# Kernel optimization log

Measured on AMD Instinct MI355X. Metric: run time of the kernel, lower is better.

Reference implementation:

```python
import jax, jax.numpy as jnp
import numpy as np
from jax import lax

K = 3        # kernel_size
PAD = 1      # padding
STRIDE = 1   # stride


def conv2d(x, w, stride, pad):
    return lax.conv_general_dilated(
        x, w, (stride, stride), [(pad, pad), (pad, pad)],
        dimension_numbers=('NCHW', 'OIHW', 'NCHW'))


def setup_inputs() -> dict:
    key = jax.random.key(0)
    ks = jax.random.split(key, 8)
    B, Ci, Cc, H, W = 8, 64, 64, 128, 128
    K2 = K * K
    return {
        'x_img': jax.random.normal(ks[0], (B, Ci, H, W), jnp.float32),
        'x_cont': jax.random.normal(ks[1], (B, Cc, H, W), jnp.float32),
        'w_fuse': jax.random.normal(ks[2], (Ci, Ci + Cc, 1, 1), jnp.float32) * 0.05,
        'w_off': jax.random.normal(ks[3], (2 * K2, Ci, K, K), jnp.float32) * 0.01,
        'b_off': jax.random.normal(ks[4], (2 * K2,), jnp.float32) * 0.1,
        'w_mod': jax.random.normal(ks[5], (K2, Ci, K, K), jnp.float32) * 0.01,
        'b_mod': jax.random.normal(ks[6], (K2,), jnp.float32) * 0.1,
        'w_reg': jax.random.normal(ks[7], (Ci, Ci, K, K), jnp.float32) * 0.05,
    }


def _bilinear_sample(img, py, px):
    # Zero padding outside the image (per-corner validity, matches torchvision).
    C, Hin, Win = img.shape
    flat = img.reshape(C, -1)
    y0 = jnp.floor(py)
    x0 = jnp.floor(px)

    def gather(yy, xx):
        valid = (yy >= 0) & (yy <= Hin - 1) & (xx >= 0) & (xx <= Win - 1)
        yc = jnp.clip(yy, 0, Hin - 1).astype(jnp.int32)
        xc = jnp.clip(xx, 0, Win - 1).astype(jnp.int32)
        return flat[:, yc * Win + xc] * valid[None].astype(img.dtype)

    wy1 = py - y0; wy0 = 1.0 - wy1
    wx1 = px - x0; wx0 = 1.0 - wx1
    return (gather(y0, x0) * (wy0 * wx0)[None]
            + gather(y0, x0 + 1.0) * (wy0 * wx1)[None]
            + gather(y0 + 1.0, x0) * (wy1 * wx0)[None]
            + gather(y0 + 1.0, x0 + 1.0) * (wy1 * wx1)[None])


def reference(x_img, x_cont, w_fuse, w_off, b_off, w_mod, b_mod, w_reg):
    # 1x1 fuse of image features with control factor
    x = conv2d(jnp.concatenate([x_img, x_cont], axis=1), w_fuse, 1, 0)
    # offset / modulator branches
    off = conv2d(x, w_off, STRIDE, PAD) + b_off[None, :, None, None]
    mod = 2.0 * jax.nn.sigmoid(conv2d(x, w_mod, STRIDE, PAD) + b_mod[None, :, None, None])
    B, C, Hin, Win = x.shape
    K2 = K * K
    Hout, Wout = off.shape[2], off.shape[3]
    # torchvision layout: channel 2k = dy, 2k+1 = dx for kernel pos k = i*K + j
    off = off.reshape(B, K2, 2, Hout, Wout)
    dy, dx = off[:, :, 0], off[:, :, 1]
    ky = (jnp.arange(K2) // K).astype(x.dtype)
    kx = (jnp.arange(K2) % K).astype(x.dtype)
    base_y = (jnp.arange(Hout) * STRIDE - PAD).astype(x.dtype)
    base_x = (jnp.arange(Wout) * STRIDE - PAD).astype(x.dtype)
    py = dy + base_y[None, None, :, None] + ky[None, :, None, None]  # [B,K2,H,W]
    px = dx + base_x[None, None, None, :] + kx[None, :, None, None]
    sampled = jax.vmap(_bilinear_sample)(x, py, px)          # [B,C,K2,H,W]
    sampled = sampled * mod[:, None]                          # modulation
    out = jnp.einsum('oik,bikhw->bohw', w_reg.reshape(C, C, K2), sampled)
    return out
```

## Files before the change

### kernel.cpp

```cpp
#include <hip/hip_runtime.h>
#include <math.h>

#define B_   8
#define C_   64
#define H_   128
#define W_   128
#define HW_  16384
#define K2_  9

typedef float f32x4 __attribute__((ext_vector_type(4)));
typedef short bf16x8 __attribute__((ext_vector_type(8)));
typedef unsigned short u16x4 __attribute__((ext_vector_type(4)));

#define WS_WRP  8192
#define WS_WRP2 26624
#define WS_XT   45056
#define WS_OM   8433664

static __device__ __forceinline__ unsigned short f2bf(float x) {
    unsigned int u = __float_as_uint(x);
    unsigned int r = (u + 0x7fffu + ((u >> 16) & 1u)) >> 16;
    return (unsigned short)r;
}
static __device__ __forceinline__ float bf2f(unsigned short u) {
    return __uint_as_float(((unsigned int)u) << 16);
}

__global__ __launch_bounds__(256) void k_fuse(const float* __restrict__ xi,
                                              const float* __restrict__ xc,
                                              const float* __restrict__ wf,
                                              const float* __restrict__ wreg,
                                              const float* __restrict__ wOff,
                                              const float* __restrict__ wMod,
                                              unsigned short* __restrict__ xtb,
                                              unsigned short* __restrict__ wrP,
                                              unsigned short* __restrict__ wrP2) {
    __shared__ unsigned short sA[1024 * 8];
    const int t = threadIdx.x;
    const int lane = t & 63;
    const int wv = t >> 6;
    const int b = blockIdx.x & 7;
    const int yh = blockIdx.x >> 3;
    const int y = yh >> 1;
    const int h = yh & 1;

    if (blockIdx.x < 18) {
        const int idx = blockIdx.x * 256 + t;
        if (idx < 4608) {
            int ln = idx & 63, mt = (idx >> 6) & 3, kc = (idx >> 8) & 1, tap = idx >> 9;
            int o = mt * 16 + (ln & 15);
            int ibase = kc * 32 + (ln >> 4) * 8;
#pragma unroll
            for (int j = 0; j < 8; ++j)
                wrP[idx * 8 + j] = f2bf(wreg[(o * 64 + ibase + j) * 9 + tap]);
        }
        if (idx < 2304) {
            int ln = idx & 63, mt = (idx >> 6) & 1, kc = idx >> 7;
            int m = mt * 16 + (ln & 15);
            int gkb = kc * 32 + (ln >> 4) * 8;
#pragma unroll
            for (int j = 0; j < 8; ++j) {
                int gk = gkb + j, tap = gk >> 6, ci = gk & 63;
                float v = 0.f;
                if (m < 18)      v = wOff[(m * 64 + ci) * 9 + tap];
                else if (m < 27) v = wMod[((m - 18) * 64 + ci) * 9 + tap];
                wrP2[idx * 8 + j] = f2bf(v);
            }
        }
    }

#pragma unroll
    for (int r = 0; r < 4; ++r) {
        const int c = t + 256 * r;
        const int f = c >> 6;
        const int ln = c & 63;
        const int mt = f & 3, kc = f >> 2;
        const int m = mt * 16 + (ln & 15);
        const int kb = kc * 32 + (ln >> 4) * 8;
        const float* s = wf + m * 128 + kb;
        unsigned short us[8];
#pragma unroll
        for (int j = 0; j < 8; ++j) us[j] = f2bf(s[j]);
        *(bf16x8*)&sA[c * 8] = *(const bf16x8*)us;
    }
    __syncthreads();

    const int n15 = lane & 15;
    const int q4 = lane >> 4;
    const int px = h * 64 + wv * 16 + n15;
    const size_t poff = (size_t)y * W_ + px;

    f32x4 acc[4];
#pragma unroll
    for (int mt = 0; mt < 4; ++mt) acc[mt] = (f32x4){0.f, 0.f, 0.f, 0.f};

#pragma unroll
    for (int kc = 0; kc < 4; ++kc) {
        const float* src = (kc < 2)
            ? (xi + ((size_t)(b * 64 + kc * 32 + q4 * 8)) * HW_ + poff)
            : (xc + ((size_t)(b * 64 + (kc - 2) * 32 + q4 * 8)) * HW_ + poff);
        unsigned short us[8];
#pragma unroll
        for (int j = 0; j < 8; ++j) us[j] = f2bf(src[(size_t)j * HW_]);
        const bf16x8 bf = *(const bf16x8*)us;
#pragma unroll
        for (int mt = 0; mt < 4; ++mt) {
            const bf16x8 a = *(const bf16x8*)&sA[((kc * 4 + mt) * 64 + lane) * 8];
            acc[mt] = __builtin_amdgcn_mfma_f32_16x16x32_bf16(a, bf, acc[mt], 0, 0, 0);
        }
    }

#pragma unroll
    for (int mt = 0; mt < 4; ++mt) {
        u16x4 o4;
        o4.x = f2bf(acc[mt][0]); o4.y = f2bf(acc[mt][1]);
        o4.z = f2bf(acc[mt][2]); o4.w = f2bf(acc[mt][3]);
        *(u16x4*)&xtb[((size_t)b * HW_ + poff) * 64 + mt * 16 + q4 * 4] = o4;
    }
}

__global__ __launch_bounds__(256) void k_offmod(const unsigned short* __restrict__ xtb,
                                                const unsigned short* __restrict__ wrP2,
                                                const float* __restrict__ bOff,
                                                const float* __restrict__ bMod,
                                                float* __restrict__ om) {
    __shared__ unsigned short sB[3 * 66 * 72];
    const int t = threadIdx.x;
    const int lane = t & 63;
    const int wv = t >> 6;
    const int b = blockIdx.x & 7;
    const int yh = blockIdx.x >> 3;
    const int y = yh >> 1;
    const int h = yh & 1;

    for (int idx = t; idx < 3 * 66 * 8; idx += 256) {
        const int c8 = idx & 7;
        const int pp = (idx >> 3) % 66;
        const int row = (idx >> 3) / 66;
        const int gx = h * 64 + pp - 1;
        const int gy = y + row - 1;
        bf16x8 v = {0, 0, 0, 0, 0, 0, 0, 0};
        if (gx >= 0 && gx < W_ && gy >= 0 && gy < H_)
            v = *(const bf16x8*)&xtb[(((size_t)(b * H_ + gy)) * W_ + gx) * 64 + c8 * 8];
        *(bf16x8*)&sB[(row * 66 + pp) * 72 + c8 * 8] = v;
    }
    __syncthreads();

    const int n15 = lane & 15;
    const int q4 = lane >> 4;

    f32x4 acc[2];
    acc[0] = (f32x4){0.f, 0.f, 0.f, 0.f};
    acc[1] = (f32x4){0.f, 0.f, 0.f, 0.f};

#pragma unroll
    for (int kc = 0; kc < 18; ++kc) {
        const int gkb = kc * 32 + q4 * 8;
        const int tap = gkb >> 6;
        const int ci = gkb & 63;
        const int row = tap / 3, kx = tap % 3;
        const bf16x8 bf = *(const bf16x8*)&sB[(row * 66 + (wv * 16 + n15 + kx)) * 72 + ci];
        const bf16x8 a0 = *(const bf16x8*)(wrP2 + (((size_t)(kc * 2 + 0) * 64 + lane) * 8));
        const bf16x8 a1 = *(const bf16x8*)(wrP2 + (((size_t)(kc * 2 + 1) * 64 + lane) * 8));
        acc[0] = __builtin_amdgcn_mfma_f32_16x16x32_bf16(a0, bf, acc[0], 0, 0, 0);
        acc[1] = __builtin_amdgcn_mfma_f32_16x16x32_bf16(a1, bf, acc[1], 0, 0, 0);
    }

    const int px = h * 64 + wv * 16 + n15;
    const size_t rec = ((size_t)(b * H_ + y)) * 28 * 128;
#pragma unroll
    for (int mt = 0; mt < 2; ++mt)
#pragma unroll
        for (int r = 0; r < 4; ++r) {
            const int o = mt * 16 + q4 * 4 + r;
            if (o < 18) {
                const int c = (o >> 1) + ((o & 1) ? 9 : 0);
                om[rec + c * 128 + px] = acc[mt][r] + bOff[o];
            } else if (o < 27) {
                const float z = acc[mt][r] + bMod[o - 18];
                om[rec + (18 + (o - 18)) * 128 + px] = 2.f / (1.f + __expf(-z));
            }
        }
}

__global__ __launch_bounds__(256) void k_deform(const unsigned short* __restrict__ xtb,
                                                const float* __restrict__ om,
                                                const unsigned short* __restrict__ wrP,
                                                float* __restrict__ out) {
    __shared__ unsigned short sS2[8 * 520];
    const int t = threadIdx.x;
    const int lane = t & 63;
    const int wv = t >> 6;
    const int b = blockIdx.x & 7;
    const int yh = blockIdx.x >> 3;
    const int y = yh >> 1;
    const int h = yh & 1;

    const char* xbB = (const char*)(xtb + (size_t)b * HW_ * 64);
    const float* omr = om + ((size_t)(b * H_ + y)) * 28 * 128;

    const int n15 = lane & 15;
    const int q4 = lane >> 4;
    const int pA = lane >> 2;
    const int corner = lane & 3;
    const int cy = corner >> 1, cx = corner & 1;
    const int pxA = h * 64 + wv * 16 + pA;
    const int gwrite = (lane >> 3) * 520 + (lane & 7);

    f32x4 acc[4];
#pragma unroll
    for (int mt = 0; mt < 4; ++mt) acc[mt] = (f32x4){0.f, 0.f, 0.f, 0.f};

    for (int k = 0; k < 9; ++k) {
        const int ky = k / 3 - 1, kx = k % 3 - 1;

        int rOff;
        int rW;
        {
            const float dy = omr[k * 128 + pxA];
            const float dxv = omr[(9 + k) * 128 + pxA];
            const float m = omr[(18 + k) * 128 + pxA];
            const float py  = (float)(y + ky) + dy;
            const float pxe = (float)(pxA + kx) + dxv;
            const float y0f = floorf(py), x0f = floorf(pxe);
            const int y0i = (int)y0f, x0i = (int)x0f;
            const float wy1 = py - y0f, wx1 = pxe - x0f;
            const int yy = y0i + cy;
            const int xx = x0i + cx;
            const bool ok = (yy >= 0) && (yy < H_) && (xx >= 0) && (xx < W_);
            const int yc = min(max(yy, 0), H_ - 1);
            const int xc = min(max(xx, 0), W_ - 1);
            const float w = (cy ? wy1 : 1.f - wy1) * (cx ? wx1 : 1.f - wx1) * m;
            rOff = (yc * W_ + xc) * 128;
            rW = (int)__float_as_uint(ok ? w : 0.f);
        }

#pragma unroll
        for (int p = 0; p < 16; ++p) {
            const int l0 = p * 4;
            const unsigned o0 = (unsigned)__builtin_amdgcn_readlane(rOff, l0 + 0);
            const unsigned o1 = (unsigned)__builtin_amdgcn_readlane(rOff, l0 + 1);
            const unsigned o2 = (unsigned)__builtin_amdgcn_readlane(rOff, l0 + 2);
            const unsigned o3 = (unsigned)__builtin_amdgcn_readlane(rOff, l0 + 3);
            const float w0 = __uint_as_float((unsigned)__builtin_amdgcn_readlane(rW, l0 + 0));
            const float w1 = __uint_as_float((unsigned)__builtin_amdgcn_readlane(rW, l0 + 1));
            const float w2 = __uint_as_float((unsigned)__builtin_amdgcn_readlane(rW, l0 + 2));
            const float w3 = __uint_as_float((unsigned)__builtin_amdgcn_readlane(rW, l0 + 3));
            const unsigned short* b0 = (const unsigned short*)(xbB + o0);
            const unsigned short* b1 = (const unsigned short*)(xbB + o1);
            const unsigned short* b2 = (const unsigned short*)(xbB + o2);
            const unsigned short* b3 = (const unsigned short*)(xbB + o3);
            const float v = bf2f(b0[lane]) * w0 + bf2f(b1[lane]) * w1
                          + bf2f(b2[lane]) * w2 + bf2f(b3[lane]) * w3;
            sS2[gwrite + (wv * 16 + p) * 8] = f2bf(v);
        }

#pragma unroll
        for (int kc = 0; kc < 2; ++kc) {
            const bf16x8 bf = *(const bf16x8*)&sS2[(kc * 4 + q4) * 520 + (wv * 16 + n15) * 8];
#pragma unroll
            for (int mt = 0; mt < 4; ++mt) {
                const bf16x8 a = *(const bf16x8*)(wrP +
                    ((((size_t)((k * 2 + kc) * 4 + mt)) * 64 + lane) * 8));
                acc[mt] = __builtin_amdgcn_mfma_f32_16x16x32_bf16(a, bf, acc[mt], 0, 0, 0);
            }
        }
    }

    const int px = h * 64 + wv * 16 + n15;
#pragma unroll
    for (int mt = 0; mt < 4; ++mt)
#pragma unroll
        for (int r = 0; r < 4; ++r) {
            const int o = mt * 16 + q4 * 4 + r;
            out[(((size_t)(b * 64 + o)) * H_ + y) * W_ + px] = acc[mt][r];
        }
}

extern "C" void kernel_launch(void* const* d_in, const int* in_sizes, int n_in,
                              void* d_out, int out_size, void* d_ws, size_t ws_size,
                              hipStream_t stream) {
    const float* x_img  = (const float*)d_in[0];
    const float* x_cont = (const float*)d_in[1];
    const float* w_fuse = (const float*)d_in[2];
    const float* w_off  = (const float*)d_in[3];
    const float* b_off  = (const float*)d_in[4];
    const float* w_mod  = (const float*)d_in[5];
    const float* b_mod  = (const float*)d_in[6];
    const float* w_reg  = (const float*)d_in[7];
    float* out = (float*)d_out;

    float* ws  = (float*)d_ws;
    unsigned short* wrP  = (unsigned short*)(ws + WS_WRP);
    unsigned short* wrP2 = (unsigned short*)(ws + WS_WRP2);
    unsigned short* xtb  = (unsigned short*)(ws + WS_XT);
    float* om  = ws + WS_OM;

    k_fuse<<<B_ * H_ * 2, 256, 0, stream>>>(x_img, x_cont, w_fuse, w_reg, w_off,
                                            w_mod, xtb, wrP, wrP2);
    k_offmod<<<B_ * H_ * 2, 256, 0, stream>>>(xtb, wrP2, b_off, b_mod, om);
    k_deform<<<B_ * H_ * 2, 256, 0, stream>>>(xtb, om, wrP, out);
}
```

Baseline: 215.7 us.

## Gather deformable samples directly into MFMA B-operand registers, dropping LDS staging

Rewrites the bilinear sampling in the deform kernel so each lane computes its own pixel's sample coordinates and loads 16-byte vectors of 8 bf16 channels per corner, matching the MFMA B-fragment layout. This replaces the scalar readlane-broadcast gather, the per-element LDS store and the LDS reload. Packed bf16 conversion now uses a single v_cvt_pk_bf16_f32 instruction. Each lane now repeats the coordinate math and holds more live registers, and the channel-sliced vector loads are less coalesced than the old per-pixel row loads.

```diff
diff --git a/kernel.cpp b/kernel.cpp
--- a/kernel.cpp
+++ b/kernel.cpp
@@ -11,6 +11,7 @@
 typedef float f32x4 __attribute__((ext_vector_type(4)));
 typedef short bf16x8 __attribute__((ext_vector_type(8)));
 typedef unsigned short u16x4 __attribute__((ext_vector_type(4)));
+typedef unsigned int u32x4 __attribute__((ext_vector_type(4)));
 
 #define WS_WRP  8192
 #define WS_WRP2 26624
@@ -24,6 +25,11 @@
 }
 static __device__ __forceinline__ float bf2f(unsigned short u) {
     return __uint_as_float(((unsigned int)u) << 16);
+}
+static __device__ __forceinline__ unsigned int cvt_pk_bf16(float lo, float hi) {
+    unsigned int r;
+    asm("v_cvt_pk_bf16_f32 %0, %1, %2" : "=v"(r) : "v"(lo), "v"(hi));
+    return r;
 }
 
 __global__ __launch_bounds__(256) void k_fuse(const float* __restrict__ xi,
@@ -187,7 +193,6 @@
                                                 const float* __restrict__ om,
                                                 const unsigned short* __restrict__ wrP,
                                                 float* __restrict__ out) {
-    __shared__ unsigned short sS2[8 * 520];
     const int t = threadIdx.x;
     const int lane = t & 63;
     const int wv = t >> 6;
@@ -201,11 +206,7 @@
 
     const int n15 = lane & 15;
     const int q4 = lane >> 4;
-    const int pA = lane >> 2;
-    const int corner = lane & 3;
-    const int cy = corner >> 1, cx = corner & 1;
-    const int pxA = h * 64 + wv * 16 + pA;
-    const int gwrite = (lane >> 3) * 520 + (lane & 7);
+    const int px = h * 64 + wv * 16 + n15;
 
     f32x4 acc[4];
 #pragma unroll
@@ -214,60 +215,70 @@
     for (int k = 0; k < 9; ++k) {
         const int ky = k / 3 - 1, kx = k % 3 - 1;
 
-        int rOff;
-        int rW;
-        {
-            const float dy = omr[k * 128 + pxA];
-            const float dxv = omr[(9 + k) * 128 + pxA];
-            const float m = omr[(18 + k) * 128 + pxA];
-            const float py  = (float)(y + ky) + dy;
-            const float pxe = (float)(pxA + kx) + dxv;
-            const float y0f = floorf(py), x0f = floorf(pxe);
-            const int y0i = (int)y0f, x0i = (int)x0f;
-            const float wy1 = py - y0f, wx1 = pxe - x0f;
+        const float dy  = omr[k * 128 + px];
+        const float dxv = omr[(9 + k) * 128 + px];
+        const float m   = omr[(18 + k) * 128 + px];
+        const float py  = (float)(y + ky) + dy;
+        const float pxe = (float)(px + kx) + dxv;
+        const float y0f = floorf(py), x0f = floorf(pxe);
+        const int y0i = (int)y0f, x0i = (int)x0f;
+        const float wy1 = py - y0f, wx1 = pxe - x0f;
+        const float wy0 = 1.f - wy1, wx0 = 1.f - wx1;
+
+        int   offs[4];
+        float wts[4];
+#pragma unroll
+        for (int c = 0; c < 4; ++c) {
+            const int cy = c >> 1, cx = c & 1;
             const int yy = y0i + cy;
             const int xx = x0i + cx;
             const bool ok = (yy >= 0) && (yy < H_) && (xx >= 0) && (xx < W_);
             const int yc = min(max(yy, 0), H_ - 1);
             const int xc = min(max(xx, 0), W_ - 1);
-            const float w = (cy ? wy1 : 1.f - wy1) * (cx ? wx1 : 1.f - wx1) * m;
-            rOff = (yc * W_ + xc) * 128;
-            rW = (int)__float_as_uint(ok ? w : 0.f);
-        }
-
-#pragma unroll
-        for (int p = 0; p < 16; ++p) {
-            const int l0 = p * 4;
-            const unsigned o0 = (unsigned)__builtin_amdgcn_readlane(rOff, l0 + 0);
-            const unsigned o1 = (unsigned)__builtin_amdgcn_readlane(rOff, l0 + 1);
-            const unsigned o2 = (unsigned)__builtin_amdgcn_readlane(rOff, l0 + 2);
-            const unsigned o3 = (unsigned)__builtin_amdgcn_readlane(rOff, l0 + 3);
-            const float w0 = __uint_as_float((unsigned)__builtin_amdgcn_readlane(rW, l0 + 0));
-            const float w1 = __uint_as_float((unsigned)__builtin_amdgcn_readlane(rW, l0 + 1));
-            const float w2 = __uint_as_float((unsigned)__builtin_amdgcn_readlane(rW, l0 + 2));
-            const float w3 = __uint_as_float((unsigned)__builtin_amdgcn_readlane(rW, l0 + 3));
-            const unsigned short* b0 = (const unsigned short*)(xbB + o0);
-            const unsigned short* b1 = (const unsigned short*)(xbB + o1);
-            const unsigned short* b2 = (const unsigned short*)(xbB + o2);
-            const unsigned short* b3 = (const unsigned short*)(xbB + o3);
-            const float v = bf2f(b0[lane]) * w0 + bf2f(b1[lane]) * w1
-                          + bf2f(b2[lane]) * w2 + bf2f(b3[lane]) * w3;
-            sS2[gwrite + (wv * 16 + p) * 8] = f2bf(v);
-        }
+            offs[c] = (yc * W_ + xc) * 128 + q4 * 16;
+            wts[c] = ok ? (cy ? wy1 : wy0) * (cx ? wx1 : wx0) * m : 0.f;
+        }
+
+        const u32x4 g00 = *(const u32x4*)(xbB + offs[0]);
+        const u32x4 g01 = *(const u32x4*)(xbB + offs[1]);
+        const u32x4 g02 = *(const u32x4*)(xbB + offs[2]);
+        const u32x4 g03 = *(const u32x4*)(xbB + offs[3]);
+        const u32x4 g10 = *(const u32x4*)(xbB + offs[0] + 64);
+        const u32x4 g11 = *(const u32x4*)(xbB + offs[1] + 64);
+        const u32x4 g12 = *(const u32x4*)(xbB + offs[2] + 64);
+        const u32x4 g13 = *(const u32x4*)(xbB + offs[3] + 64);
+
+        const float w0 = wts[0], w1 = wts[1], w2 = wts[2], w3 = wts[3];
 
 #pragma unroll
         for (int kc = 0; kc < 2; ++kc) {
-            const bf16x8 bf = *(const bf16x8*)&sS2[(kc * 4 + q4) * 520 + (wv * 16 + n15) * 8];
+            const u32x4 c0 = kc ? g10 : g00;
+            const u32x4 c1 = kc ? g11 : g01;
+            const u32x4 c2 = kc ? g12 : g02;
+            const u32x4 c3 = kc ? g13 : g03;
+            unsigned int outw[4];
+#pragma unroll
+            for (int d = 0; d < 4; ++d) {
+                const float lo = __uint_as_float(c0[d] << 16) * w0
+                               + __uint_as_float(c1[d] << 16) * w1
+                               + __uint_as_float(c2[d] << 16) * w2
+                               + __uint_as_float(c3[d] << 16) * w3;
+                const float hi = __uint_as_float(c0[d] & 0xffff0000u) * w0
+                               + __uint_as_float(c1[d] & 0xffff0000u) * w1
+                               + __uint_as_float(c2[d] & 0xffff0000u) * w2
+                               + __uint_as_float(c3[d] & 0xffff0000u) * w3;
+                outw[d] = cvt_pk_bf16(lo, hi);
+            }
+            const bf16x8 bfB = *(const bf16x8*)outw;
 #pragma unroll
             for (int mt = 0; mt < 4; ++mt) {
                 const bf16x8 a = *(const bf16x8*)(wrP +
                     ((((size_t)((k * 2 + kc) * 4 + mt)) * 64 + lane) * 8));
-                acc[mt] = __builtin_amdgcn_mfma_f32_16x16x32_bf16(a, bf, acc[mt], 0, 0, 0);
+                acc[mt] = __builtin_amdgcn_mfma_f32_16x16x32_bf16(a, bfB, acc[mt], 0, 0, 0);
             }
         }
     }
 
-    const int px = h * 64 + wv * 16 + n15;
 #pragma unroll
     for (int mt = 0; mt < 4; ++mt)
 #pragma unroll
```

New measurement: 222.9 us. 1.03x slower.
